# Optimization experiments

Hardware: AMD Instinct MI355X
Metric: run time of the kernel (lower is better)

The kernel has to match this reference:

```python
import jax, jax.numpy as jnp
import numpy as np
from jax import lax

NUM_CLASSES = 21
MAX_OUT = 5          # max_output_size in tf.image.non_max_suppression
IOU_THR = 0.5        # NMS_IOU_THRESHOLD
CONF_THR = 0.5       # CONFIDENCE_THRESHOLD
NEG = -1e9           # stand-in for -inf score (suppressed / background)


def setup_inputs() -> dict:
    key = jax.random.key(0)
    k1, k2, k3 = jax.random.split(key, 3)
    B, N, C = 128, 8732, NUM_CLASSES
    logits = jax.random.normal(k1, (B, N, 4 + C), dtype=jnp.float32)
    # default boxes in corner format [ymin, xmin, ymax, xmax], valid geometry
    ctr = jax.random.uniform(k2, (N, 2), dtype=jnp.float32)                 # cy, cx
    sz = jax.random.uniform(k3, (N, 2), dtype=jnp.float32, minval=0.05, maxval=0.3)  # h, w
    default_boxes = jnp.clip(
        jnp.concatenate([ctr - sz / 2, ctr + sz / 2], axis=-1), 0.0, 1.0)
    return {"logits": logits, "default_boxes": default_boxes}


def _decode(loc, db):
    # db: [N,4] corners -> center/size (matches get_offset's tf.stack)
    cy = (db[:, 2] + db[:, 0]) / 2
    cx = (db[:, 3] + db[:, 1]) / 2
    h = db[:, 2] - db[:, 0]
    w = db[:, 3] - db[:, 1]
    # loc: [B,N,4] = (dy, dx, dh, dw)
    ncy = loc[..., 0] * h + cy
    ncx = loc[..., 1] * w + cx
    nh = jnp.exp(loc[..., 2]) * h
    nw = jnp.exp(loc[..., 3]) * w
    boxes = jnp.stack(
        [ncy - nh / 2, ncx - nw / 2, ncy + nh / 2, ncx + nw / 2], axis=-1)
    return jnp.clip(boxes, 0.0, 1.0)


def _iou_one_vs_all(box, boxes):
    # box [4], boxes [N,4], corner format
    tl = jnp.maximum(box[:2], boxes[:, :2])
    br = jnp.minimum(box[2:], boxes[:, 2:])
    wh = jnp.maximum(br - tl, 0.0)
    inter = wh[:, 0] * wh[:, 1]
    a1 = (box[2] - box[0]) * (box[3] - box[1])
    a2 = (boxes[:, 2] - boxes[:, 0]) * (boxes[:, 3] - boxes[:, 1])
    return inter / (a1 + a2 - inter + 1e-12)


def _nms_single(boxes, scores, classes_f):
    # boxes [N,4], scores [N] (background already set to NEG), classes_f [N] float
    def step(s, _):
        i = jnp.argmax(s)
        sc = s[i]
        b = boxes[i]
        valid = sc > CONF_THR  # score_threshold in tf NMS
        iou = _iou_one_vs_all(b, boxes)
        s = jnp.where(iou > IOU_THR, NEG, s)  # suppresses i too (IoU=1)
        return s, (b, classes_f[i], sc, valid)

    _, (bs, cs, ss, vs) = lax.scan(step, scores, None, length=MAX_OUT)
    # pad invalid slots with zeros (TF returns variable-length; we use fixed 5 + zero pad)
    bs = jnp.where(vs[:, None], bs, 0.0)
    cs = jnp.where(vs, cs, 0.0)
    ss = jnp.where(vs, ss, 0.0)
    return bs, cs[:, None], ss[:, None]  # [5,4], [5,1], [5,1]


def reference(logits, default_boxes):
    boxes = _decode(logits[..., :4], default_boxes)          # [B,N,4]
    probs = jax.nn.softmax(logits[..., 4:], axis=-1)         # [B,N,C]
    scores = jnp.max(probs, axis=-1)                          # [B,N]
    classes = jnp.argmax(probs, axis=-1)                      # [B,N] int
    # boolean_mask(classes != 0) expressed as score = -inf for background
    scores_eff = jnp.where(classes != 0, scores, NEG)
    det_b, det_c, det_s = jax.vmap(_nms_single)(
        boxes, scores_eff, classes.astype(jnp.float32))
    # pack detection_boxes / detection_classes / detection_scores -> [B,5,6]
    return jnp.concatenate([det_b, det_c, det_s], axis=-1)
```

## Files before the change

kernel.cpp:

```cpp
#include <hip/hip_runtime.h>

#define NEG (-1e9f)
constexpr int NCLS   = 21;
constexpr int NBOX   = 8732;
constexpr int MAXOUT = 5;
constexpr int CAP    = NBOX;
constexpr float IOU_THR  = 0.5f;
constexpr float CONF_THR = 0.5f;

__global__ __launch_bounds__(256) void decode_kernel(
        const float* __restrict__ logits,
        const float* __restrict__ dbox,
        float4* __restrict__ cand,
        int* __restrict__ cnt,
        int BN) {
    __shared__ float sl[256 * 25];
    const int t = threadIdx.x;
    const long long baseF = (long long)blockIdx.x * (256 * 25);
    const long long totalF = (long long)BN * 25;

    const float4* gl = (const float4*)(logits + baseF);
    float4* sl4 = (float4*)sl;
    for (int j = t; j < 1600; j += 256) {
        if (baseF + (long long)j * 4 + 3 < totalF) sl4[j] = gl[j];
    }
    __syncthreads();

    const int i = blockIdx.x * 256 + t;
    if (i >= BN) return;
    const float* L = sl + t * 25;
    const int n = i % NBOX;
    const int b = i / NBOX;

    float d0 = dbox[n * 4 + 0], d1 = dbox[n * 4 + 1];
    float d2 = dbox[n * 4 + 2], d3 = dbox[n * 4 + 3];
    float cy = (d2 + d0) * 0.5f;
    float cx = (d3 + d1) * 0.5f;
    float h  = d2 - d0;
    float w  = d3 - d1;
    float ncy = L[0] * h + cy;
    float ncx = L[1] * w + cx;
    float nh  = expf(L[2]) * h;
    float nw  = expf(L[3]) * w;
    float y1 = fminf(fmaxf(ncy - nh * 0.5f, 0.f), 1.f);
    float x1 = fminf(fmaxf(ncx - nw * 0.5f, 0.f), 1.f);
    float y2 = fminf(fmaxf(ncy + nh * 0.5f, 0.f), 1.f);
    float x2 = fminf(fmaxf(ncx + nw * 0.5f, 0.f), 1.f);

    float m = L[4];
    int am = 0;
#pragma unroll
    for (int j = 1; j < NCLS; j++) {
        float x = L[4 + j];
        if (x > m) { m = x; am = j; }
    }
    float sum = 0.f;
#pragma unroll
    for (int j = 0; j < NCLS; j++) sum += expf(L[4 + j] - m);
    float score = 1.0f / sum;

    if (am != 0 && score > CONF_THR) {
        int p = atomicAdd(&cnt[b], 1);
        if (p < CAP) {
            float4* c = cand + ((long long)b * CAP + p) * 2;
            c[0] = make_float4(y1, x1, y2, x2);
            c[1] = make_float4(score, (float)am, (float)n, 0.f);
        }
    }
}

__global__ __launch_bounds__(256) void nms_kernel(
        const float4* __restrict__ cand,
        const int* __restrict__ cnt,
        float* __restrict__ out) {
    const int b = blockIdx.x;
    const int t = threadIdx.x;
    __shared__ float s_sc[CAP];
    __shared__ float s_id[CAP];
    __shared__ float r_v[256];
    __shared__ float r_oid[256];
    __shared__ int   r_i[256];
    __shared__ float4 selbox_sh;

    const int M = min(cnt[b], CAP);
    const float4* cb = cand + (long long)b * CAP * 2;

    for (int i = t; i < M; i += 256) {
        float4 mrec = cb[i * 2 + 1];
        s_sc[i] = mrec.x;
        s_id[i] = mrec.z;
    }
    __syncthreads();

    for (int k = 0; k < MAXOUT; k++) {
        float bv = -INFINITY, boid = 3.0e38f;
        int bi = -1;
        for (int i = t; i < M; i += 256) {
            float v = s_sc[i], oid = s_id[i];
            if (v > bv || (v == bv && oid < boid)) { bv = v; boid = oid; bi = i; }
        }
        r_v[t] = bv; r_oid[t] = boid; r_i[t] = bi;
        __syncthreads();
        for (int off = 128; off > 0; off >>= 1) {
            if (t < off) {
                float v2 = r_v[t + off];
                if (v2 > r_v[t] || (v2 == r_v[t] && r_oid[t + off] < r_oid[t])) {
                    r_v[t] = v2; r_oid[t] = r_oid[t + off]; r_i[t] = r_i[t + off];
                }
            }
            __syncthreads();
        }
        const int   sel = r_i[0];
        const float sc  = r_v[0];
        const bool valid = (sel >= 0) && (sc > CONF_THR);

        if (t == 0) {
            float* o = out + ((long long)b * MAXOUT + k) * 6;
            if (valid) {
                float4 bx = cb[sel * 2];
                float4 mm = cb[sel * 2 + 1];
                selbox_sh = bx;
                o[0] = bx.x; o[1] = bx.y; o[2] = bx.z; o[3] = bx.w;
                o[4] = mm.y; o[5] = sc;
            } else {
                o[0] = 0.f; o[1] = 0.f; o[2] = 0.f;
                o[3] = 0.f; o[4] = 0.f; o[5] = 0.f;
            }
        }
        __syncthreads();
        if (!valid) continue;

        float4 sb = selbox_sh;
        float a1 = (sb.z - sb.x) * (sb.w - sb.y);
        for (int i = t; i < M; i += 256) {
            float4 c = cb[i * 2];
            float tly = fmaxf(sb.x, c.x);
            float tlx = fmaxf(sb.y, c.y);
            float bry = fminf(sb.z, c.z);
            float brx = fminf(sb.w, c.w);
            float wh0 = fmaxf(bry - tly, 0.f);
            float wh1 = fmaxf(brx - tlx, 0.f);
            float inter = wh0 * wh1;
            float a2 = (c.z - c.x) * (c.w - c.y);
            float iou = inter / (a1 + a2 - inter + 1e-12f);
            if (iou > IOU_THR) s_sc[i] = NEG;
        }
        __syncthreads();
    }
}

extern "C" void kernel_launch(void* const* d_in, const int* in_sizes, int n_in,
                              void* d_out, int out_size, void* d_ws, size_t ws_size,
                              hipStream_t stream) {
    const float* logits = (const float*)d_in[0];
    const float* dbox   = (const float*)d_in[1];
    float* out          = (float*)d_out;

    const int N  = in_sizes[1] / 4;
    const int B  = in_sizes[0] / (N * 25);
    const int BN = B * N;

    int* cnt = (int*)d_ws;
    float4* cand = (float4*)((char*)d_ws + (((size_t)B * sizeof(int) + 15) & ~(size_t)15));

    hipMemsetAsync(cnt, 0, (size_t)B * sizeof(int), stream);
    decode_kernel<<<(BN + 255) / 256, 256, 0, stream>>>(logits, dbox, cand, cnt, BN);
    nms_kernel<<<B, 256, 0, stream>>>(cand, cnt, out);
}
```

Measured before the change: 207.0 us.

## Use per-wave direct-to-LDS loads in decode and single-wave NMS with shuffles

```diff
diff --git a/kernel.cpp b/kernel.cpp
--- a/kernel.cpp
+++ b/kernel.cpp
@@ -10,34 +10,50 @@
 
 __global__ __launch_bounds__(256) void decode_kernel(
         const float* __restrict__ logits,
-        const float* __restrict__ dbox,
+        const float4* __restrict__ dbox4,
         float4* __restrict__ cand,
         int* __restrict__ cnt,
         int BN) {
-    __shared__ float sl[256 * 25];
-    const int t = threadIdx.x;
-    const long long baseF = (long long)blockIdx.x * (256 * 25);
+    __shared__ float sl[4][64 * 25];
+    const int t    = threadIdx.x;
+    const int wave = t >> 6;
+    const int lane = t & 63;
+    float* slw = sl[wave];
+
+    const long long waveBox = ((long long)blockIdx.x * 4 + wave) * 64;
+    if (waveBox >= BN) return;
+    const long long gF     = waveBox * 25;
     const long long totalF = (long long)BN * 25;
 
-    const float4* gl = (const float4*)(logits + baseF);
-    float4* sl4 = (float4*)sl;
-    for (int j = t; j < 1600; j += 256) {
-        if (baseF + (long long)j * 4 + 3 < totalF) sl4[j] = gl[j];
+    if (waveBox + 64 <= BN) {
+        const float* gbase = logits + gF;
+#pragma unroll
+        for (int c = 0; c < 25; c++) {
+            __builtin_amdgcn_global_load_lds(
+                (const __attribute__((address_space(1))) void*)(gbase + c * 64 + lane),
+                (__attribute__((address_space(3))) void*)(slw + c * 64),
+                4, 0, 0);
+        }
+    } else {
+        for (int j = lane; j < 64 * 25; j += 64) {
+            long long g = gF + j;
+            slw[j] = (g < totalF) ? logits[g] : 0.f;
+        }
     }
-    __syncthreads();
+    __builtin_amdgcn_s_waitcnt(0x0F70);
+    __builtin_amdgcn_sched_barrier(0);
 
-    const int i = blockIdx.x * 256 + t;
+    const long long i = waveBox + lane;
     if (i >= BN) return;
-    const float* L = sl + t * 25;
-    const int n = i % NBOX;
-    const int b = i / NBOX;
+    const float* L = slw + lane * 25;
+    const int n = (int)(i % NBOX);
+    const int b = (int)(i / NBOX);
 
-    float d0 = dbox[n * 4 + 0], d1 = dbox[n * 4 + 1];
-    float d2 = dbox[n * 4 + 2], d3 = dbox[n * 4 + 3];
-    float cy = (d2 + d0) * 0.5f;
-    float cx = (d3 + d1) * 0.5f;
-    float h  = d2 - d0;
-    float w  = d3 - d1;
+    float4 db = dbox4[n];
+    float cy = (db.z + db.x) * 0.5f;
+    float cx = (db.w + db.y) * 0.5f;
+    float h  = db.z - db.x;
+    float w  = db.w - db.y;
     float ncy = L[0] * h + cy;
     float ncx = L[1] * w + cx;
     float nh  = expf(L[2]) * h;
@@ -69,70 +85,51 @@
     }
 }
 
-__global__ __launch_bounds__(256) void nms_kernel(
+__global__ __launch_bounds__(64) void nms_kernel(
         const float4* __restrict__ cand,
         const int* __restrict__ cnt,
         float* __restrict__ out) {
-    const int b = blockIdx.x;
-    const int t = threadIdx.x;
+    const int b    = blockIdx.x;
+    const int lane = threadIdx.x;
     __shared__ float s_sc[CAP];
     __shared__ float s_id[CAP];
-    __shared__ float r_v[256];
-    __shared__ float r_oid[256];
-    __shared__ int   r_i[256];
-    __shared__ float4 selbox_sh;
 
     const int M = min(cnt[b], CAP);
     const float4* cb = cand + (long long)b * CAP * 2;
+    float* o = out + (long long)b * MAXOUT * 6;
 
-    for (int i = t; i < M; i += 256) {
+    for (int i = lane; i < M; i += 64) {
         float4 mrec = cb[i * 2 + 1];
         s_sc[i] = mrec.x;
         s_id[i] = mrec.z;
     }
-    __syncthreads();
 
-    for (int k = 0; k < MAXOUT; k++) {
+    int k = 0;
+    for (; k < MAXOUT; k++) {
         float bv = -INFINITY, boid = 3.0e38f;
         int bi = -1;
-        for (int i = t; i < M; i += 256) {
+        for (int i = lane; i < M; i += 64) {
             float v = s_sc[i], oid = s_id[i];
             if (v > bv || (v == bv && oid < boid)) { bv = v; boid = oid; bi = i; }
         }
-        r_v[t] = bv; r_oid[t] = boid; r_i[t] = bi;
-        __syncthreads();
-        for (int off = 128; off > 0; off >>= 1) {
-            if (t < off) {
-                float v2 = r_v[t + off];
-                if (v2 > r_v[t] || (v2 == r_v[t] && r_oid[t + off] < r_oid[t])) {
-                    r_v[t] = v2; r_oid[t] = r_oid[t + off]; r_i[t] = r_i[t + off];
-                }
-            }
-            __syncthreads();
+        for (int mm = 32; mm >= 1; mm >>= 1) {
+            float v2 = __shfl_xor(bv,   mm, 64);
+            float o2 = __shfl_xor(boid, mm, 64);
+            int   i2 = __shfl_xor(bi,   mm, 64);
+            if (v2 > bv || (v2 == bv && o2 < boid)) { bv = v2; boid = o2; bi = i2; }
         }
-        const int   sel = r_i[0];
-        const float sc  = r_v[0];
-        const bool valid = (sel >= 0) && (sc > CONF_THR);
+        if (bi < 0 || !(bv > CONF_THR)) break;
 
-        if (t == 0) {
-            float* o = out + ((long long)b * MAXOUT + k) * 6;
-            if (valid) {
-                float4 bx = cb[sel * 2];
-                float4 mm = cb[sel * 2 + 1];
-                selbox_sh = bx;
-                o[0] = bx.x; o[1] = bx.y; o[2] = bx.z; o[3] = bx.w;
-                o[4] = mm.y; o[5] = sc;
-            } else {
-                o[0] = 0.f; o[1] = 0.f; o[2] = 0.f;
-                o[3] = 0.f; o[4] = 0.f; o[5] = 0.f;
-            }
+        float4 sb = cb[bi * 2];
+        if (lane == 0) {
+            float4 mm2 = cb[bi * 2 + 1];
+            o[k * 6 + 0] = sb.x; o[k * 6 + 1] = sb.y;
+            o[k * 6 + 2] = sb.z; o[k * 6 + 3] = sb.w;
+            o[k * 6 + 4] = mm2.y; o[k * 6 + 5] = bv;
         }
-        __syncthreads();
-        if (!valid) continue;
 
-        float4 sb = selbox_sh;
         float a1 = (sb.z - sb.x) * (sb.w - sb.y);
-        for (int i = t; i < M; i += 256) {
+        for (int i = lane; i < M; i += 64) {
             float4 c = cb[i * 2];
             float tly = fmaxf(sb.x, c.x);
             float tlx = fmaxf(sb.y, c.y);
@@ -145,15 +142,15 @@
             float iou = inter / (a1 + a2 - inter + 1e-12f);
             if (iou > IOU_THR) s_sc[i] = NEG;
         }
-        __syncthreads();
     }
+    for (int j = k * 6 + lane; j < MAXOUT * 6; j += 64) o[j] = 0.f;
 }
 
 extern "C" void kernel_launch(void* const* d_in, const int* in_sizes, int n_in,
                               void* d_out, int out_size, void* d_ws, size_t ws_size,
                               hipStream_t stream) {
     const float* logits = (const float*)d_in[0];
-    const float* dbox   = (const float*)d_in[1];
+    const float4* dbox4 = (const float4*)d_in[1];
     float* out          = (float*)d_out;
 
     const int N  = in_sizes[1] / 4;
@@ -164,6 +161,6 @@
     float4* cand = (float4*)((char*)d_ws + (((size_t)B * sizeof(int) + 15) & ~(size_t)15));
 
     hipMemsetAsync(cnt, 0, (size_t)B * sizeof(int), stream);
-    decode_kernel<<<(BN + 255) / 256, 256, 0, stream>>>(logits, dbox, cand, cnt, BN);
-    nms_kernel<<<B, 256, 0, stream>>>(cand, cnt, out);
+    decode_kernel<<<(BN + 255) / 256, 256, 0, stream>>>(logits, dbox4, cand, cnt, BN);
+    nms_kernel<<<B, 64, 0, stream>>>(cand, cnt, out);
 }
```

After: 194.8 us. 5.9% less time.
